# Performance work log

Measured on AMD Instinct MI355X. Metric: run time of the kernel, lower is better.

Reference implementation:

```python
import jax, jax.numpy as jnp
import numpy as np

N_NODES = 50000
N_EDGES = 800000
IN_DIM = 256
HIDDEN = 32
HEADS = 4
OUT_DIM = 2
NEG_SLOPE = 0.2  # PyG GATConv default LeakyReLU slope


def setup_inputs() -> dict:
    key = jax.random.key(0)
    ks = jax.random.split(key, 12)
    s = 0.05
    return {
        "x": jax.random.normal(ks[0], (N_NODES, IN_DIM), dtype=jnp.float32),
        "edge_index": jax.random.randint(ks[1], (2, N_EDGES), 0, N_NODES, dtype=jnp.int32),
        # conv1: in_dim -> hidden, heads=4, concat
        "W1": jax.random.normal(ks[2], (IN_DIM, HEADS * HIDDEN), dtype=jnp.float32) * s,
        "att_src1": jax.random.normal(ks[3], (HEADS, HIDDEN), dtype=jnp.float32) * s,
        "att_dst1": jax.random.normal(ks[4], (HEADS, HIDDEN), dtype=jnp.float32) * s,
        "b1": jnp.zeros((HEADS * HIDDEN,), dtype=jnp.float32),
        # conv2: heads*hidden -> hidden, heads=1, mean (concat=False)
        "W2": jax.random.normal(ks[5], (HEADS * HIDDEN, 1 * HIDDEN), dtype=jnp.float32) * s,
        "att_src2": jax.random.normal(ks[6], (1, HIDDEN), dtype=jnp.float32) * s,
        "att_dst2": jax.random.normal(ks[7], (1, HIDDEN), dtype=jnp.float32) * s,
        "b2": jnp.zeros((HIDDEN,), dtype=jnp.float32),
        # final classifier
        "lin_w": jax.random.normal(ks[8], (HIDDEN, OUT_DIM), dtype=jnp.float32) * s,
        "lin_b": jnp.zeros((OUT_DIM,), dtype=jnp.float32),
    }


def gat_conv(x, src, dst, W, att_src, att_dst, bias, concat):
    """PyG-style GATConv (v1), eval mode (no dropout), self-loops already in src/dst."""
    N = x.shape[0]
    H, C = att_src.shape
    h = (x @ W).reshape(N, H, C)                       # [N,H,C]
    a_s = jnp.sum(h * att_src, axis=-1)                # [N,H]
    a_d = jnp.sum(h * att_dst, axis=-1)                # [N,H]
    e = jax.nn.leaky_relu(a_s[src] + a_d[dst], NEG_SLOPE)  # [E,H]
    # numerically-stable softmax over edges grouped by destination node
    m = jax.ops.segment_max(e, dst, num_segments=N)    # [N,H]
    p = jnp.exp(e - m[dst])
    denom = jax.ops.segment_sum(p, dst, num_segments=N)
    alpha = p / denom[dst]                             # [E,H]
    out = jax.ops.segment_sum(alpha[:, :, None] * h[src], dst, num_segments=N)  # [N,H,C]
    out = out.reshape(N, H * C) if concat else out.mean(axis=1)
    return out + bias


def reference(x, edge_index, W1, att_src1, att_dst1, b1, W2, att_src2, att_dst2, b2, lin_w, lin_b):
    N = x.shape[0]
    loops = jnp.arange(N, dtype=edge_index.dtype)      # PyG default add_self_loops=True
    src = jnp.concatenate([edge_index[0], loops])
    dst = jnp.concatenate([edge_index[1], loops])
    h = jax.nn.elu(gat_conv(x, src, dst, W1, att_src1, att_dst1, b1, concat=True))
    h = jax.nn.elu(gat_conv(h, src, dst, W2, att_src2, att_dst2, b2, concat=False))
    return h @ lin_w + lin_b
```

## Files before the change

kernel.cpp:

```cpp
#include <hip/hip_runtime.h>
#include <hip/hip_fp16.h>

#define IN_DIM 256
#define HID 32
#define HEADS 4
#define F1 128
#define BSHIFT 9
#define MAXBUK 128

static __device__ __forceinline__ float leaky(float x){ return x > 0.f ? x : 0.2f*x; }
static __device__ __forceinline__ float elu(float x){ return x > 0.f ? x : (__expf(x) - 1.f); }

static __device__ __forceinline__ unsigned short f2bf(float f){
  unsigned int u = __float_as_uint(f);
  u += 0x7FFFu + ((u >> 16) & 1u);
  return (unsigned short)(u >> 16);
}
static __device__ __forceinline__ float bf2f(unsigned short h){
  return __uint_as_float(((unsigned int)h) << 16);
}
static __device__ __forceinline__ unsigned int pack2(unsigned short a, unsigned short b){
  return (unsigned int)a | ((unsigned int)b << 16);
}
static __device__ __forceinline__ unsigned short f2h(float f){
  return __half_as_ushort(__float2half(f));
}
static __device__ __forceinline__ float hlo(unsigned int u){
  return __half2float(__ushort_as_half((unsigned short)(u & 0xFFFFu)));
}
static __device__ __forceinline__ float hhi(unsigned int u){
  return __half2float(__ushort_as_half((unsigned short)(u >> 16)));
}

__device__ __forceinline__ int block_excl_scan(int v, int tid, int* total){
  __shared__ int ws[8];
  int lane = tid & 63, w = tid >> 6;
  int incl = v;
  #pragma unroll
  for (int d = 1; d < 64; d <<= 1){ int o = __shfl_up(incl, d); if (lane >= d) incl += o; }
  if (lane == 63) ws[w] = incl;
  __syncthreads();
  if (tid == 0){ int s = 0; for (int i = 0; i < 4; ++i){ int t = ws[i]; ws[i] = s; s += t; } ws[4] = s; }
  __syncthreads();
  *total = ws[4];
  int e = ws[w] + incl - v;
  __syncthreads();
  return e;
}

__global__ __launch_bounds__(256) void bukcnt_kernel(const int* __restrict__ dsts,
    int* __restrict__ cnt_blk, int E, int nbuk, int stride){
  __shared__ int lcnt[MAXBUK];
  int tid = threadIdx.x, blk = blockIdx.x;
  if (tid < nbuk) lcnt[tid] = 0;
  __syncthreads();
  int base = blk*2048;
  #pragma unroll
  for (int j = 0; j < 8; ++j){
    int i = base + tid + j*256;
    if (i < E) atomicAdd(&lcnt[dsts[i] >> BSHIFT], 1);
  }
  __syncthreads();
  if (tid < nbuk) cnt_blk[tid*stride + blk] = lcnt[tid];
}

__global__ __launch_bounds__(256) void bukscan1_kernel(int* __restrict__ cnt_blk,
    int* __restrict__ btot, int nchk, int stride){
  int b = blockIdx.x, tid = threadIdx.x;
  int carry = 0;
  for (int s = 0; s < nchk; s += 256){
    int i = s + tid;
    int v = (i < nchk) ? cnt_blk[b*stride + i] : 0;
    int tot; int e = block_excl_scan(v, tid, &tot);
    if (i < nchk) cnt_blk[b*stride + i] = carry + e;
    carry += tot;
  }
  if (tid == 0) btot[b] = carry;
}

__global__ __launch_bounds__(256) void bukscan2_kernel(const int* __restrict__ btot,
    int* __restrict__ bucket_base, int* __restrict__ offs, int nbuk, int Nn, int E){
  int tid = threadIdx.x;
  int v = (tid < nbuk) ? btot[tid] : 0;
  int tot; int e = block_excl_scan(v, tid, &tot);
  if (tid <= nbuk) bucket_base[tid] = e;
  if (tid == 0) offs[Nn] = E;
}

__global__ __launch_bounds__(256) void bukscat_kernel(const int* __restrict__ srcs,
    const int* __restrict__ dsts, const int* __restrict__ cnt_blk,
    const int* __restrict__ bucket_base, unsigned int* __restrict__ im,
    int E, int nbuk, int stride){
  __shared__ int lcur[MAXBUK];
  int tid = threadIdx.x, blk = blockIdx.x;
  if (tid < nbuk) lcur[tid] = bucket_base[tid] + cnt_blk[tid*stride + blk];
  __syncthreads();
  int base = blk*2048;
  #pragma unroll
  for (int j = 0; j < 8; ++j){
    int i = base + tid + j*256;
    if (i < E){
      int s = srcs[i], d = dsts[i];
      int r = atomicAdd(&lcur[d >> BSHIFT], 1);
      im[r] = (unsigned)s | (((unsigned)d & 511u) << 16);
    }
  }
}

__global__ __launch_bounds__(256) void bukfine_kernel(const unsigned int* __restrict__ im,
    const int* __restrict__ bucket_base, int* __restrict__ offs, int* __restrict__ csr, int Nn){
  __shared__ int lcnt[512], lpfx[512];
  int b = blockIdx.x, tid = threadIdx.x;
  int node0 = b << BSHIFT;
  int nn = min(512, Nn - node0);
  lcnt[tid] = 0; lcnt[tid+256] = 0;
  __syncthreads();
  int ebeg = bucket_base[b], eend = bucket_base[b+1];
  for (int i = ebeg + tid; i < eend; i += 256)
    atomicAdd(&lcnt[im[i] >> 16], 1);
  __syncthreads();
  int carry = 0;
  for (int s = 0; s < 512; s += 256){
    int v = lcnt[s + tid];
    int tot; int e = block_excl_scan(v, tid, &tot);
    lpfx[s + tid] = carry + e;
    carry += tot;
  }
  __syncthreads();
  if (tid < nn) offs[node0 + tid] = ebeg + lpfx[tid];
  if (tid + 256 < nn) offs[node0 + tid + 256] = ebeg + lpfx[tid + 256];
  lcnt[tid] = ebeg + lpfx[tid];
  lcnt[tid+256] = ebeg + lpfx[tid+256];
  __syncthreads();
  for (int i = ebeg + tid; i < eend; i += 256){
    unsigned int u = im[i];
    int pos = atomicAdd(&lcnt[u >> 16], 1);
    csr[pos] = (int)(u & 0xFFFFu);
  }
}

__global__ __launch_bounds__(256) void convw_kernel(const float* __restrict__ W1,
    unsigned short* __restrict__ Wh, unsigned short* __restrict__ Wl){
  int i = blockIdx.x*256 + threadIdx.x;
  int n = i >> 8, k = i & 255;
  float w = W1[(size_t)k*F1 + n];
  unsigned short h = f2bf(w);
  Wh[i] = h;
  Wl[i] = f2bf(w - bf2f(h));
}

typedef __attribute__((ext_vector_type(8))) short bf8_t;
typedef __attribute__((ext_vector_type(4))) float f4_t;

__global__ __launch_bounds__(256) void gemm1_kernel(const float* __restrict__ x,
    const unsigned short* __restrict__ Wh, const unsigned short* __restrict__ Wl,
    const float* __restrict__ att_src, const float* __restrict__ att_dst,
    unsigned short* __restrict__ h1b, float* __restrict__ as1, float* __restrict__ ad1, int M){
  __shared__ uint4 AhV[64][5], AlV[64][5];
  __shared__ uint4 BhV[128][5], BlV[128][5];
  const int tid = threadIdx.x;
  const int m0 = blockIdx.x*64;
  const int wave = tid >> 6, lane = tid & 63;
  const int quad = lane >> 4, l16 = lane & 15;
  const int wr = (wave & 1)*32;
  const int wc = (wave >> 1)*64;
  f4_t acc[2][4];
  #pragma unroll
  for (int r = 0; r < 2; ++r)
    #pragma unroll
    for (int c = 0; c < 4; ++c)
      #pragma unroll
      for (int i = 0; i < 4; ++i) acc[r][c][i] = 0.f;

  const int ar = tid >> 2, akc = tid & 3;
  const bool aok = (m0 + ar) < M;
  const float* ap = x + (size_t)(m0 + ar)*IN_DIM + 8*akc;
  const int bn = tid >> 1, bkc = (tid & 1)*2;
  const unsigned short* bph = Wh + (size_t)bn*256 + 16*(tid & 1);
  const unsigned short* bpl = Wl + (size_t)bn*256 + 16*(tid & 1);

  for (int k0 = 0; k0 < IN_DIM; k0 += 32){
    float4 a0 = make_float4(0.f,0.f,0.f,0.f), a1 = a0;
    if (aok){ a0 = *(const float4*)(ap + k0); a1 = *(const float4*)(ap + k0 + 4); }
    float v[8] = {a0.x,a0.y,a0.z,a0.w,a1.x,a1.y,a1.z,a1.w};
    unsigned short hh[8], ll[8];
    #pragma unroll
    for (int j = 0; j < 8; ++j){
      unsigned short h = f2bf(v[j]); hh[j] = h; ll[j] = f2bf(v[j] - bf2f(h));
    }
    uint4 hv; hv.x = pack2(hh[0],hh[1]); hv.y = pack2(hh[2],hh[3]); hv.z = pack2(hh[4],hh[5]); hv.w = pack2(hh[6],hh[7]);
    uint4 lv; lv.x = pack2(ll[0],ll[1]); lv.y = pack2(ll[2],ll[3]); lv.z = pack2(ll[4],ll[5]); lv.w = pack2(ll[6],ll[7]);
    AhV[ar][akc] = hv;
    AlV[ar][akc] = lv;
    BhV[bn][bkc+0] = *(const uint4*)(bph + k0);
    BhV[bn][bkc+1] = *(const uint4*)(bph + k0 + 8);
    BlV[bn][bkc+0] = *(const uint4*)(bpl + k0);
    BlV[bn][bkc+1] = *(const uint4*)(bpl + k0 + 8);
    __syncthreads();

    bf8_t arh[2], arl[2], brh[4], brl[4];
    #pragma unroll
    for (int r = 0; r < 2; ++r){
      arh[r] = *(const bf8_t*)&AhV[wr + r*16 + l16][quad];
      arl[r] = *(const bf8_t*)&AlV[wr + r*16 + l16][quad];
    }
    #pragma unroll
    for (int c = 0; c < 4; ++c){
      brh[c] = *(const bf8_t*)&BhV[wc + c*16 + l16][quad];
      brl[c] = *(const bf8_t*)&BlV[wc + c*16 + l16][quad];
    }
    #pragma unroll
    for (int r = 0; r < 2; ++r)
      #pragma unroll
      for (int c = 0; c < 4; ++c){
        acc[r][c] = __builtin_amdgcn_mfma_f32_16x16x32_bf16(arh[r], brh[c], acc[r][c], 0, 0, 0);
        acc[r][c] = __builtin_amdgcn_mfma_f32_16x16x32_bf16(arh[r], brl[c], acc[r][c], 0, 0, 0);
        acc[r][c] = __builtin_amdgcn_mfma_f32_16x16x32_bf16(arl[r], brh[c], acc[r][c], 0, 0, 0);
      }
    __syncthreads();
  }

  const int head0 = wc >> 5;
  float sv[4], dv[4];
  #pragma unroll
  for (int c = 0; c < 4; ++c){
    int col_in_head = (c & 1)*16 + l16;
    sv[c] = att_src[(head0 + (c >> 1))*HID + col_in_head];
    dv[c] = att_dst[(head0 + (c >> 1))*HID + col_in_head];
  }
  #pragma unroll
  for (int r = 0; r < 2; ++r){
    #pragma unroll
    for (int i = 0; i < 4; ++i){
      int row = m0 + wr + r*16 + quad*4 + i;
      bool ok = row < M;
      float hv0 = acc[r][0][i], hv1 = acc[r][1][i], hv2 = acc[r][2][i], hv3 = acc[r][3][i];
      if (ok){
        unsigned short* hp = h1b + (size_t)row*F1 + wc + l16;
        hp[0]  = f2h(hv0); hp[16] = f2h(hv1); hp[32] = f2h(hv2); hp[48] = f2h(hv3);
      }
      float p0 = hv0*sv[0] + hv1*sv[1];
      float p1 = hv2*sv[2] + hv3*sv[3];
      float q0 = hv0*dv[0] + hv1*dv[1];
      float q1 = hv2*dv[2] + hv3*dv[3];
      p0 += __shfl_xor(p0,1); p0 += __shfl_xor(p0,2); p0 += __shfl_xor(p0,4); p0 += __shfl_xor(p0,8);
      p1 += __shfl_xor(p1,1); p1 += __shfl_xor(p1,2); p1 += __shfl_xor(p1,4); p1 += __shfl_xor(p1,8);
      q0 += __shfl_xor(q0,1); q0 += __shfl_xor(q0,2); q0 += __shfl_xor(q0,4); q0 += __shfl_xor(q0,8);
      q1 += __shfl_xor(q1,1); q1 += __shfl_xor(q1,2); q1 += __shfl_xor(q1,4); q1 += __shfl_xor(q1,8);
      if (ok && l16 == 0){
        as1[row*4 + head0]     = p0;
        as1[row*4 + head0 + 1] = p1;
        ad1[row*4 + head0]     = q0;
        ad1[row*4 + head0 + 1] = q1;
      }
    }
  }
}

__global__ __launch_bounds__(256) void agg1_kernel(const unsigned int* __restrict__ h1b,
    const float* __restrict__ a_s1, const float* __restrict__ a_d1,
    const int* __restrict__ offs, const int* __restrict__ csr,
    const float* __restrict__ b1, uint4* __restrict__ h1a4, int N){
  int n = blockIdx.x*4 + (threadIdx.x >> 6);
  if (n >= N) return;
  const int lane = threadIdx.x & 63;
  const int sub  = lane >> 4;
  const int cl   = lane & 15;
  const int head = cl >> 2;
  const int j    = cl & 3;
  const int pbase = (lane & ~15) + (head << 2);
  const float ad = a_d1[n*4+head];
  const int cw = 4*cl;
  float a0=0,a1=0,a2=0,a3=0,a4=0,a5=0,a6=0,a7=0,den=0;
  if (sub == 0){
    float p = __expf(leaky(a_s1[n*4+head] + ad));
    uint4 u = *(const uint4*)(h1b + (size_t)n*64 + cw);
    a0 = p*hlo(u.x); a1 = p*hhi(u.x); a2 = p*hlo(u.y); a3 = p*hhi(u.y);
    a4 = p*hlo(u.z); a5 = p*hhi(u.z); a6 = p*hlo(u.w); a7 = p*hhi(u.w);
    den = p;
  }
  const int beg = offs[n], end = offs[n+1];
  int e = beg + sub;
  for (; e + 12 < end; e += 16){
    int s0 = csr[e], s1 = csr[e+4], s2 = csr[e+8], s3 = csr[e+12];
    int sown = j == 0 ? s0 : (j == 1 ? s1 : (j == 2 ? s2 : s3));
    float pown = __expf(leaky(a_s1[sown*4+head] + ad));
    float p0 = __shfl(pown, pbase+0);
    float p1 = __shfl(pown, pbase+1);
    float p2 = __shfl(pown, pbase+2);
    float p3 = __shfl(pown, pbase+3);
    uint4 u0 = *(const uint4*)(h1b + (size_t)s0*64 + cw);
    uint4 u1 = *(const uint4*)(h1b + (size_t)s1*64 + cw);
    uint4 u2 = *(const uint4*)(h1b + (size_t)s2*64 + cw);
    uint4 u3 = *(const uint4*)(h1b + (size_t)s3*64 + cw);
    a0 += p0*hlo(u0.x) + p1*hlo(u1.x) + p2*hlo(u2.x) + p3*hlo(u3.x);
    a1 += p0*hhi(u0.x) + p1*hhi(u1.x) + p2*hhi(u2.x) + p3*hhi(u3.x);
    a2 += p0*hlo(u0.y) + p1*hlo(u1.y) + p2*hlo(u2.y) + p3*hlo(u3.y);
    a3 += p0*hhi(u0.y) + p1*hhi(u1.y) + p2*hhi(u2.y) + p3*hhi(u3.y);
    a4 += p0*hlo(u0.z) + p1*hlo(u1.z) + p2*hlo(u2.z) + p3*hlo(u3.z);
    a5 += p0*hhi(u0.z) + p1*hhi(u1.z) + p2*hhi(u2.z) + p3*hhi(u3.z);
    a6 += p0*hlo(u0.w) + p1*hlo(u1.w) + p2*hlo(u2.w) + p3*hlo(u3.w);
    a7 += p0*hhi(u0.w) + p1*hhi(u1.w) + p2*hhi(u2.w) + p3*hhi(u3.w);
    den += p0 + p1 + p2 + p3;
  }
  for (; e < end; e += 4){
    int s = csr[e];
    float p = __expf(leaky(a_s1[s*4+head] + ad));
    uint4 u = *(const uint4*)(h1b + (size_t)s*64 + cw);
    a0 += p*hlo(u.x); a1 += p*hhi(u.x); a2 += p*hlo(u.y); a3 += p*hhi(u.y);
    a4 += p*hlo(u.z); a5 += p*hhi(u.z); a6 += p*hlo(u.w); a7 += p*hhi(u.w);
    den += p;
  }
  #pragma unroll
  for (int off = 16; off < 64; off <<= 1){
    a0 += __shfl_xor(a0,off); a1 += __shfl_xor(a1,off);
    a2 += __shfl_xor(a2,off); a3 += __shfl_xor(a3,off);
    a4 += __shfl_xor(a4,off); a5 += __shfl_xor(a5,off);
    a6 += __shfl_xor(a6,off); a7 += __shfl_xor(a7,off);
    den += __shfl_xor(den,off);
  }
  if (sub == 0){
    float inv = 1.f/den;
    int ch = 8*cl;
    float4 b0 = *(const float4*)(b1 + ch);
    float4 b4 = *(const float4*)(b1 + ch + 4);
    uint4 w;
    w.x = pack2(f2h(elu(a0*inv+b0.x)), f2h(elu(a1*inv+b0.y)));
    w.y = pack2(f2h(elu(a2*inv+b0.z)), f2h(elu(a3*inv+b0.w)));
    w.z = pack2(f2h(elu(a4*inv+b4.x)), f2h(elu(a5*inv+b4.y)));
    w.w = pack2(f2h(elu(a6*inv+b4.z)), f2h(elu(a7*inv+b4.w)));
    h1a4[(size_t)n*16 + cl] = w;
  }
}

__global__ __launch_bounds__(256) void gemm2_kernel(const uint4* __restrict__ h1a4, const float* __restrict__ W2,
    const float* __restrict__ att_src, const float* __restrict__ att_dst,
    unsigned int* __restrict__ h2b, float* __restrict__ as2, float* __restrict__ ad2, int M){
  __shared__ float As[64*132];
  __shared__ float Ws[128*32];
  const int tid = threadIdx.x;
  const int cg = tid & 15;
  const int rg = tid >> 4;
  const int m0 = blockIdx.x*64;
  #pragma unroll
  for (int p = 0; p < 4; ++p){
    int jj = tid + 256*p;
    int r = jj >> 4, q = jj & 15;
    int row = m0 + r;
    uint4 u = make_uint4(0,0,0,0);
    if (row < M) u = h1a4[(size_t)row*16 + q];
    float4 f0 = make_float4(hlo(u.x), hhi(u.x), hlo(u.y), hhi(u.y));
    float4 f1 = make_float4(hlo(u.z), hhi(u.z), hlo(u.w), hhi(u.w));
    *(float4*)&As[r*132 + 8*q]     = f0;
    *(float4*)&As[r*132 + 8*q + 4] = f1;
  }
  #pragma unroll
  for (int p = 0; p < 4; ++p){
    int i = tid + 256*p;
    ((float4*)Ws)[i] = ((const float4*)W2)[i];
  }
  __syncthreads();
  float acc[4][2] = {};
  const float* a0p = &As[(4*rg+0)*132];
  const float* a1p = &As[(4*rg+1)*132];
  const float* a2p = &As[(4*rg+2)*132];
  const float* a3p = &As[(4*rg+3)*132];
  #pragma unroll 8
  for (int kk = 0; kk < 128; ++kk){
    float2 w = *(const float2*)&Ws[kk*32 + 2*cg];
    float a0 = a0p[kk], a1 = a1p[kk], a2 = a2p[kk], a3 = a3p[kk];
    acc[0][0]+=a0*w.x; acc[0][1]+=a0*w.y;
    acc[1][0]+=a1*w.x; acc[1][1]+=a1*w.y;
    acc[2][0]+=a2*w.x; acc[2][1]+=a2*w.y;
    acc[3][0]+=a3*w.x; acc[3][1]+=a3*w.y;
  }
  const float2 sv = *(const float2*)(att_src + 2*cg);
  const float2 dv = *(const float2*)(att_dst + 2*cg);
  #pragma unroll
  for (int i = 0; i < 4; ++i){
    int row = m0 + 4*rg + i;
    if (row < M){
      float2 o = make_float2(acc[i][0], acc[i][1]);
      h2b[(size_t)row*16 + cg] = pack2(f2h(o.x), f2h(o.y));
      float ps = o.x*sv.x + o.y*sv.y;
      float pd = o.x*dv.x + o.y*dv.y;
      ps += __shfl_xor(ps,1); ps += __shfl_xor(ps,2); ps += __shfl_xor(ps,4); ps += __shfl_xor(ps,8);
      pd += __shfl_xor(pd,1); pd += __shfl_xor(pd,2); pd += __shfl_xor(pd,4); pd += __shfl_xor(pd,8);
      if (cg == 0){ as2[row] = ps; ad2[row] = pd; }
    }
  }
}

__global__ __launch_bounds__(256) void agg2_kernel(const unsigned int* __restrict__ h2b,
    const float* __restrict__ as2, const float* __restrict__ ad2,
    const int* __restrict__ offs, const int* __restrict__ csr,
    const float* __restrict__ b2, const float* __restrict__ linw, const float* __restrict__ linb,
    float* __restrict__ out, int N){
  int n = blockIdx.x*4 + (threadIdx.x >> 6);
  if (n >= N) return;
  const int lane = threadIdx.x & 63;
  const int sub  = lane >> 3;
  const int cl   = lane & 7;
  const int j    = cl & 3;
  const int pbase = lane & ~7;
  const int cw   = 2*cl;
  const float ad = ad2[n];
  float a0=0,a1=0,a2=0,a3=0,den=0;
  if (sub == 0){
    float p = __expf(leaky(as2[n] + ad));
    uint2 u = *(const uint2*)(h2b + (size_t)n*16 + cw);
    a0 = p*hlo(u.x); a1 = p*hhi(u.x); a2 = p*hlo(u.y); a3 = p*hhi(u.y);
    den = p;
  }
  const int beg = offs[n], end = offs[n+1];
  int e = beg + sub;
  for (; e + 24 < end; e += 32){
    int s0 = csr[e], s1 = csr[e+8], s2 = csr[e+16], s3 = csr[e+24];
    int sown = j == 0 ? s0 : (j == 1 ? s1 : (j == 2 ? s2 : s3));
    float pown = __expf(leaky(as2[sown] + ad));
    float p0 = __shfl(pown, pbase+0);
    float p1 = __shfl(pown, pbase+1);
    float p2 = __shfl(pown, pbase+2);
    float p3 = __shfl(pown, pbase+3);
    uint2 u0 = *(const uint2*)(h2b + (size_t)s0*16 + cw);
    uint2 u1 = *(const uint2*)(h2b + (size_t)s1*16 + cw);
    uint2 u2 = *(const uint2*)(h2b + (size_t)s2*16 + cw);
    uint2 u3 = *(const uint2*)(h2b + (size_t)s3*16 + cw);
    a0 += p0*hlo(u0.x) + p1*hlo(u1.x) + p2*hlo(u2.x) + p3*hlo(u3.x);
    a1 += p0*hhi(u0.x) + p1*hhi(u1.x) + p2*hhi(u2.x) + p3*hhi(u3.x);
    a2 += p0*hlo(u0.y) + p1*hlo(u1.y) + p2*hlo(u2.y) + p3*hlo(u3.y);
    a3 += p0*hhi(u0.y) + p1*hhi(u1.y) + p2*hhi(u2.y) + p3*hhi(u3.y);
    den += p0 + p1 + p2 + p3;
  }
  for (; e < end; e += 8){
    int s = csr[e];
    float p = __expf(leaky(as2[s] + ad));
    uint2 u = *(const uint2*)(h2b + (size_t)s*16 + cw);
    a0 += p*hlo(u.x); a1 += p*hhi(u.x); a2 += p*hlo(u.y); a3 += p*hhi(u.y);
    den += p;
  }
  #pragma unroll
  for (int off = 8; off < 64; off <<= 1){
    a0 += __shfl_xor(a0,off); a1 += __shfl_xor(a1,off);
    a2 += __shfl_xor(a2,off); a3 += __shfl_xor(a3,off);
    den += __shfl_xor(den,off);
  }
  float inv = 1.f/den;
  int ch = 4*cl;
  float o0 = elu(a0*inv + b2[ch+0]);
  float o1 = elu(a1*inv + b2[ch+1]);
  float o2 = elu(a2*inv + b2[ch+2]);
  float o3 = elu(a3*inv + b2[ch+3]);
  float r0 = o0*linw[2*(ch+0)]   + o1*linw[2*(ch+1)]   + o2*linw[2*(ch+2)]   + o3*linw[2*(ch+3)];
  float r1 = o0*linw[2*(ch+0)+1] + o1*linw[2*(ch+1)+1] + o2*linw[2*(ch+2)+1] + o3*linw[2*(ch+3)+1];
  r0 += __shfl_xor(r0,1); r0 += __shfl_xor(r0,2); r0 += __shfl_xor(r0,4);
  r1 += __shfl_xor(r1,1); r1 += __shfl_xor(r1,2); r1 += __shfl_xor(r1,4);
  if (lane == 0){
    out[(size_t)n*2+0] = r0 + linb[0];
    out[(size_t)n*2+1] = r1 + linb[1];
  }
}

extern "C" void kernel_launch(void* const* d_in, const int* in_sizes, int n_in,
                              void* d_out, int out_size, void* d_ws, size_t ws_size,
                              hipStream_t stream) {
  const float* x    = (const float*)d_in[0];
  const int*   ei   = (const int*)  d_in[1];
  const float* W1   = (const float*)d_in[2];
  const float* as1w = (const float*)d_in[3];
  const float* ad1w = (const float*)d_in[4];
  const float* b1   = (const float*)d_in[5];
  const float* W2   = (const float*)d_in[6];
  const float* as2w = (const float*)d_in[7];
  const float* ad2w = (const float*)d_in[8];
  const float* b2   = (const float*)d_in[9];
  const float* linw = (const float*)d_in[10];
  const float* linb = (const float*)d_in[11];
  float* out = (float*)d_out;

  const int N = in_sizes[0] / IN_DIM;
  const int E = in_sizes[1] / 2;

  const int NBUK = (N + 511) >> BSHIFT;
  const int NCHK = (E + 2047) / 2048;
  const int CSTR = (NCHK + 3) & ~3;

  char* ws = (char*)d_ws;
  auto alloc = [&](size_t bytes) -> char* {
    char* p = ws; ws += (bytes + 255) & ~(size_t)255; return p;
  };
  unsigned short* h1b = (unsigned short*)alloc((size_t)N*F1*2);
  uint4* h1a4 = (uint4*)alloc((size_t)N*F1*2);
  unsigned int* h2b = (unsigned int*)alloc((size_t)N*HID*2);
  float* a_s1 = (float*)alloc((size_t)N*4*4);
  float* a_d1 = (float*)alloc((size_t)N*4*4);
  float* a_s2 = (float*)alloc((size_t)N*4);
  float* a_d2 = (float*)alloc((size_t)N*4);
  size_t cntblk_bytes = (size_t)NBUK*CSTR*4;
  if (cntblk_bytes < 131072) cntblk_bytes = 131072;
  int* cnt_blk = (int*)alloc(cntblk_bytes);
  int* btot    = (int*)alloc((size_t)(NBUK+1)*4);
  int* bbase   = (int*)alloc((size_t)(NBUK+1)*4);
  int* offs    = (int*)alloc((size_t)(N+1)*4);
  int* csr     = (int*)alloc((size_t)E*4);
  unsigned int* im = (unsigned int*)h1b;
  unsigned short* W1h = (unsigned short*)cnt_blk;
  unsigned short* W1l = W1h + (size_t)IN_DIM*F1;

  const int* srcs = ei;
  const int* dsts = ei + E;

  bukcnt_kernel<<<NCHK, 256, 0, stream>>>(dsts, cnt_blk, E, NBUK, CSTR);
  bukscan1_kernel<<<NBUK, 256, 0, stream>>>(cnt_blk, btot, NCHK, CSTR);
  bukscan2_kernel<<<1, 256, 0, stream>>>(btot, bbase, offs, NBUK, N, E);
  bukscat_kernel<<<NCHK, 256, 0, stream>>>(srcs, dsts, cnt_blk, bbase, im, E, NBUK, CSTR);
  bukfine_kernel<<<NBUK, 256, 0, stream>>>(im, bbase, offs, csr, N);
  convw_kernel<<<(IN_DIM*F1)/256, 256, 0, stream>>>(W1, W1h, W1l);
  gemm1_kernel<<<(N+63)/64, 256, 0, stream>>>(x, W1h, W1l, as1w, ad1w, h1b, a_s1, a_d1, N);
  agg1_kernel<<<(N+3)/4, 256, 0, stream>>>((const unsigned int*)h1b, a_s1, a_d1, offs, csr, b1, h1a4, N);
  gemm2_kernel<<<(N+63)/64, 256, 0, stream>>>(h1a4, W2, as2w, ad2w, h2b, a_s2, a_d2, N);
  agg2_kernel<<<(N+3)/4, 256, 0, stream>>>(h2b, a_s2, a_d2, offs, csr, b2, linw, linb, out, N);
}
```

Before: 242.8 us.

## Use f16 MFMA with hi/lo split for gemm2 and fuse W1 conversion

```diff
diff --git a/kernel.cpp b/kernel.cpp
--- a/kernel.cpp
+++ b/kernel.cpp
@@ -49,9 +49,19 @@
 }
 
 __global__ __launch_bounds__(256) void bukcnt_kernel(const int* __restrict__ dsts,
-    int* __restrict__ cnt_blk, int E, int nbuk, int stride){
+    int* __restrict__ cnt_blk, const float* __restrict__ W1,
+    unsigned short* __restrict__ Wh, unsigned short* __restrict__ Wl,
+    int E, int nbuk, int stride){
   __shared__ int lcnt[MAXBUK];
   int tid = threadIdx.x, blk = blockIdx.x;
+  int gid = blk*256 + tid;
+  if (gid < IN_DIM*F1){
+    int n = gid >> 8, k = gid & 255;
+    float w = W1[(size_t)k*F1 + n];
+    unsigned short h = f2bf(w);
+    Wh[gid] = h;
+    Wl[gid] = f2bf(w - bf2f(h));
+  }
   if (tid < nbuk) lcnt[tid] = 0;
   __syncthreads();
   int base = blk*2048;
@@ -139,18 +149,9 @@
   }
 }
 
-__global__ __launch_bounds__(256) void convw_kernel(const float* __restrict__ W1,
-    unsigned short* __restrict__ Wh, unsigned short* __restrict__ Wl){
-  int i = blockIdx.x*256 + threadIdx.x;
-  int n = i >> 8, k = i & 255;
-  float w = W1[(size_t)k*F1 + n];
-  unsigned short h = f2bf(w);
-  Wh[i] = h;
-  Wl[i] = f2bf(w - bf2f(h));
-}
-
 typedef __attribute__((ext_vector_type(8))) short bf8_t;
 typedef __attribute__((ext_vector_type(4))) float f4_t;
+typedef _Float16 f16x8 __attribute__((ext_vector_type(8)));
 
 __global__ __launch_bounds__(256) void gemm1_kernel(const float* __restrict__ x,
     const unsigned short* __restrict__ Wh, const unsigned short* __restrict__ Wl,
@@ -335,59 +336,79 @@
 
 __global__ __launch_bounds__(256) void gemm2_kernel(const uint4* __restrict__ h1a4, const float* __restrict__ W2,
     const float* __restrict__ att_src, const float* __restrict__ att_dst,
-    unsigned int* __restrict__ h2b, float* __restrict__ as2, float* __restrict__ ad2, int M){
-  __shared__ float As[64*132];
-  __shared__ float Ws[128*32];
+    unsigned short* __restrict__ h2s, float* __restrict__ as2, float* __restrict__ ad2, int M){
+  __shared__ unsigned short Ab[64*136];
+  __shared__ unsigned short Bh[32*136];
+  __shared__ unsigned short Bl[32*136];
   const int tid = threadIdx.x;
-  const int cg = tid & 15;
-  const int rg = tid >> 4;
   const int m0 = blockIdx.x*64;
+  const int wave = tid >> 6, lane = tid & 63;
+  const int quad = lane >> 4, l16 = lane & 15;
+
   #pragma unroll
   for (int p = 0; p < 4; ++p){
-    int jj = tid + 256*p;
-    int r = jj >> 4, q = jj & 15;
+    int idx = tid + 256*p;
+    int r = idx >> 4, q = idx & 15;
     int row = m0 + r;
     uint4 u = make_uint4(0,0,0,0);
     if (row < M) u = h1a4[(size_t)row*16 + q];
-    float4 f0 = make_float4(hlo(u.x), hhi(u.x), hlo(u.y), hhi(u.y));
-    float4 f1 = make_float4(hlo(u.z), hhi(u.z), hlo(u.w), hhi(u.w));
-    *(float4*)&As[r*132 + 8*q]     = f0;
-    *(float4*)&As[r*132 + 8*q + 4] = f1;
-  }
-  #pragma unroll
-  for (int p = 0; p < 4; ++p){
-    int i = tid + 256*p;
-    ((float4*)Ws)[i] = ((const float4*)W2)[i];
-  }
-  __syncthreads();
-  float acc[4][2] = {};
-  const float* a0p = &As[(4*rg+0)*132];
-  const float* a1p = &As[(4*rg+1)*132];
-  const float* a2p = &As[(4*rg+2)*132];
-  const float* a3p = &As[(4*rg+3)*132];
-  #pragma unroll 8
-  for (int kk = 0; kk < 128; ++kk){
-    float2 w = *(const float2*)&Ws[kk*32 + 2*cg];
-    float a0 = a0p[kk], a1 = a1p[kk], a2 = a2p[kk], a3 = a3p[kk];
-    acc[0][0]+=a0*w.x; acc[0][1]+=a0*w.y;
-    acc[1][0]+=a1*w.x; acc[1][1]+=a1*w.y;
-    acc[2][0]+=a2*w.x; acc[2][1]+=a2*w.y;
-    acc[3][0]+=a3*w.x; acc[3][1]+=a3*w.y;
-  }
-  const float2 sv = *(const float2*)(att_src + 2*cg);
-  const float2 dv = *(const float2*)(att_dst + 2*cg);
+    *(uint4*)&Ab[r*136 + 8*q] = u;
+  }
+  {
+    const float4* w4 = (const float4*)W2;
+    #pragma unroll
+    for (int p = 0; p < 4; ++p){
+      int idx = tid*4 + p;
+      float4 v = w4[idx];
+      int e0 = idx*4;
+      float vv[4] = {v.x, v.y, v.z, v.w};
+      #pragma unroll
+      for (int t = 0; t < 4; ++t){
+        int e = e0 + t, k = e >> 5, n = e & 31;
+        __half hi = __float2half(vv[t]);
+        __half lo = __float2half((vv[t] - __half2float(hi)) * 4096.f);
+        Bh[n*136 + k] = __half_as_ushort(hi);
+        Bl[n*136 + k] = __half_as_ushort(lo);
+      }
+    }
+  }
+  __syncthreads();
+
+  f4_t acch[2], accl[2];
+  #pragma unroll
+  for (int c = 0; c < 2; ++c)
+    #pragma unroll
+    for (int i = 0; i < 4; ++i){ acch[c][i] = 0.f; accl[c][i] = 0.f; }
+
+  #pragma unroll
+  for (int kc = 0; kc < 4; ++kc){
+    f16x8 a = *(const f16x8*)&Ab[(16*wave + l16)*136 + kc*32 + quad*8];
+    #pragma unroll
+    for (int c = 0; c < 2; ++c){
+      f16x8 bh = *(const f16x8*)&Bh[(16*c + l16)*136 + kc*32 + quad*8];
+      f16x8 bl = *(const f16x8*)&Bl[(16*c + l16)*136 + kc*32 + quad*8];
+      acch[c] = __builtin_amdgcn_mfma_f32_16x16x32_f16(a, bh, acch[c], 0, 0, 0);
+      accl[c] = __builtin_amdgcn_mfma_f32_16x16x32_f16(a, bl, accl[c], 0, 0, 0);
+    }
+  }
+
+  const float sv0 = att_src[l16],      dv0 = att_dst[l16];
+  const float sv1 = att_src[l16 + 16], dv1 = att_dst[l16 + 16];
   #pragma unroll
   for (int i = 0; i < 4; ++i){
-    int row = m0 + 4*rg + i;
-    if (row < M){
-      float2 o = make_float2(acc[i][0], acc[i][1]);
-      h2b[(size_t)row*16 + cg] = pack2(f2h(o.x), f2h(o.y));
-      float ps = o.x*sv.x + o.y*sv.y;
-      float pd = o.x*dv.x + o.y*dv.y;
-      ps += __shfl_xor(ps,1); ps += __shfl_xor(ps,2); ps += __shfl_xor(ps,4); ps += __shfl_xor(ps,8);
-      pd += __shfl_xor(pd,1); pd += __shfl_xor(pd,2); pd += __shfl_xor(pd,4); pd += __shfl_xor(pd,8);
-      if (cg == 0){ as2[row] = ps; ad2[row] = pd; }
-    }
+    int row = m0 + 16*wave + quad*4 + i;
+    bool ok = row < M;
+    float v0 = acch[0][i] + accl[0][i] * (1.f/4096.f);
+    float v1 = acch[1][i] + accl[1][i] * (1.f/4096.f);
+    if (ok){
+      h2s[(size_t)row*32 + l16]      = f2h(v0);
+      h2s[(size_t)row*32 + l16 + 16] = f2h(v1);
+    }
+    float ps = v0*sv0 + v1*sv1;
+    float pd = v0*dv0 + v1*dv1;
+    ps += __shfl_xor(ps,1); ps += __shfl_xor(ps,2); ps += __shfl_xor(ps,4); ps += __shfl_xor(ps,8);
+    pd += __shfl_xor(pd,1); pd += __shfl_xor(pd,2); pd += __shfl_xor(pd,4); pd += __shfl_xor(pd,8);
+    if (ok && l16 == 0){ as2[row] = ps; ad2[row] = pd; }
   }
 }
 
@@ -491,33 +512,30 @@
   };
   unsigned short* h1b = (unsigned short*)alloc((size_t)N*F1*2);
   uint4* h1a4 = (uint4*)alloc((size_t)N*F1*2);
-  unsigned int* h2b = (unsigned int*)alloc((size_t)N*HID*2);
+  unsigned short* h2s = (unsigned short*)alloc((size_t)N*HID*2);
   float* a_s1 = (float*)alloc((size_t)N*4*4);
   float* a_d1 = (float*)alloc((size_t)N*4*4);
   float* a_s2 = (float*)alloc((size_t)N*4);
   float* a_d2 = (float*)alloc((size_t)N*4);
-  size_t cntblk_bytes = (size_t)NBUK*CSTR*4;
-  if (cntblk_bytes < 131072) cntblk_bytes = 131072;
-  int* cnt_blk = (int*)alloc(cntblk_bytes);
+  int* cnt_blk = (int*)alloc((size_t)NBUK*CSTR*4);
   int* btot    = (int*)alloc((size_t)(NBUK+1)*4);
   int* bbase   = (int*)alloc((size_t)(NBUK+1)*4);
   int* offs    = (int*)alloc((size_t)(N+1)*4);
   int* csr     = (int*)alloc((size_t)E*4);
-  unsigned int* im = (unsigned int*)h1b;
-  unsigned short* W1h = (unsigned short*)cnt_blk;
-  unsigned short* W1l = W1h + (size_t)IN_DIM*F1;
+  unsigned int* im = (unsigned int*)alloc((size_t)E*4);
+  unsigned short* W1h = (unsigned short*)alloc((size_t)IN_DIM*F1*2);
+  unsigned short* W1l = (unsigned short*)alloc((size_t)IN_DIM*F1*2);
 
   const int* srcs = ei;
   const int* dsts = ei + E;
 
-  bukcnt_kernel<<<NCHK, 256, 0, stream>>>(dsts, cnt_blk, E, NBUK, CSTR);
+  bukcnt_kernel<<<NCHK, 256, 0, stream>>>(dsts, cnt_blk, W1, W1h, W1l, E, NBUK, CSTR);
   bukscan1_kernel<<<NBUK, 256, 0, stream>>>(cnt_blk, btot, NCHK, CSTR);
   bukscan2_kernel<<<1, 256, 0, stream>>>(btot, bbase, offs, NBUK, N, E);
   bukscat_kernel<<<NCHK, 256, 0, stream>>>(srcs, dsts, cnt_blk, bbase, im, E, NBUK, CSTR);
   bukfine_kernel<<<NBUK, 256, 0, stream>>>(im, bbase, offs, csr, N);
-  convw_kernel<<<(IN_DIM*F1)/256, 256, 0, stream>>>(W1, W1h, W1l);
   gemm1_kernel<<<(N+63)/64, 256, 0, stream>>>(x, W1h, W1l, as1w, ad1w, h1b, a_s1, a_d1, N);
   agg1_kernel<<<(N+3)/4, 256, 0, stream>>>((const unsigned int*)h1b, a_s1, a_d1, offs, csr, b1, h1a4, N);
-  gemm2_kernel<<<(N+63)/64, 256, 0, stream>>>(h1a4, W2, as2w, ad2w, h2b, a_s2, a_d2, N);
-  agg2_kernel<<<(N+3)/4, 256, 0, stream>>>(h2b, a_s2, a_d2, offs, csr, b2, linw, linb, out, N);
-}
+  gemm2_kernel<<<(N+63)/64, 256, 0, stream>>>(h1a4, W2, as2w, ad2w, h2s, a_s2, a_d2, N);
+  agg2_kernel<<<(N+3)/4, 256, 0, stream>>>((const unsigned int*)h2s, a_s2, a_d2, offs, csr, b2, linw, linb, out, N);
+}
```

Measured after the change: 233.0 us. -4.0%, faster.
